# Kernel optimization log

Hardware: AMD Instinct MI355X
Metric: run time of the kernel (lower is better)

Reference implementation:

```python
import jax, jax.numpy as jnp
import numpy as np

B, N, D, S, K = 32, 2048, 512, 2, 1024
DS = D // S  # slice_dim = 256
BETA = 0.25


def setup_inputs() -> dict:
    key = jax.random.key(0)
    k1, k2 = jax.random.split(key)
    h = jax.random.normal(k1, (B, N, D), dtype=jnp.float32)
    # torch init: uniform(-1/K, 1/K) per codebook
    W = jax.random.uniform(k2, (S, K, DS), dtype=jnp.float32,
                           minval=-1.0 / K, maxval=1.0 / K)
    return {"h": h, "W": W}


def reference(h, W):
    Bb, Nn, Dd = h.shape
    Ss, Kk, Ds = W.shape
    # [S, B*N, Ds] sliced views of h
    x = h.reshape(Bb * Nn, Ss, Ds).transpose(1, 0, 2)
    # squared euclidean distances per slice: [S, BN, K]
    x_sq = jnp.sum(x * x, axis=-1, keepdims=True)
    w_sq = jnp.sum(W * W, axis=-1)  # [S, K]
    dist = x_sq + w_sq[:, None, :] - 2.0 * jnp.einsum('smd,skd->smk', x, W)
    ids = jnp.argmin(dist, axis=-1)  # [S, BN]
    # gather codebook vectors per slice
    z_q = jax.vmap(lambda w, i: w[i])(W, ids)  # [S, BN, Ds]
    # per-slice VQ losses (mean over BN*Ds elements), summed over slices
    cb = jnp.mean((z_q - jax.lax.stop_gradient(x)) ** 2, axis=(1, 2))
    cm = jnp.mean((x - jax.lax.stop_gradient(z_q)) ** 2, axis=(1, 2))
    vq_total = jnp.sum(cb + BETA * cm)
    # straight-through estimator
    z_st = x + jax.lax.stop_gradient(z_q - x)  # [S, BN, Ds]
    z = z_st.transpose(1, 0, 2).reshape(Bb, Nn, Dd)
    # pack slice ids: offsets = [1, K, K^2, ...]
    offs = (Kk ** jnp.arange(Ss)).astype(jnp.int32)
    ids_packed = jnp.sum(ids.astype(jnp.int32) * offs[:, None], axis=0).reshape(Bb, Nn)
    return z, ids_packed, vq_total
```

## Files before the change

### kernel.cpp

```cpp
#include <hip/hip_runtime.h>

#define BN_   65536
#define K_    1024
#define DS_   256
#define D_    512
#define TM    64
#define TK    128

__global__ __launch_bounds__(256)
void wsq_kernel(const float* __restrict__ W, float* __restrict__ wsq) {
  const int k = blockIdx.x * 256 + threadIdx.x;
  const float4* row = (const float4*)(W + (size_t)k * DS_);
  float s0 = 0.f, s1 = 0.f, s2 = 0.f, s3 = 0.f;
#pragma unroll
  for (int i = 0; i < DS_ / 4; ++i) {
    const float4 v = row[i];
    s0 = fmaf(v.x, v.x, s0);
    s1 = fmaf(v.y, v.y, s1);
    s2 = fmaf(v.z, v.z, s2);
    s3 = fmaf(v.w, v.w, s3);
  }
  wsq[k] = (s0 + s1) + (s2 + s3);
}

__global__ __launch_bounds__(256)
void xsq_kernel(const float* __restrict__ h, float* __restrict__ xsq) {
  const int idx = blockIdx.x * 256 + threadIdx.x;
  const int s = idx >> 16;
  const int m = idx & 0xFFFF;
  const float* x = h + (size_t)m * D_ + s * DS_;
  float blk[2];
#pragma unroll
  for (int b = 0; b < 2; ++b) {
    const float* a = x + b * 128;
    float r[8];
#pragma unroll
    for (int j = 0; j < 8; ++j) r[j] = __fmul_rn(a[j], a[j]);
    for (int t = 1; t < 16; ++t) {
#pragma unroll
      for (int j = 0; j < 8; ++j) {
        const float p = __fmul_rn(a[t * 8 + j], a[t * 8 + j]);
        r[j] = __fadd_rn(r[j], p);
      }
    }
    const float s01 = __fadd_rn(r[0], r[1]);
    const float s23 = __fadd_rn(r[2], r[3]);
    const float s45 = __fadd_rn(r[4], r[5]);
    const float s67 = __fadd_rn(r[6], r[7]);
    blk[b] = __fadd_rn(__fadd_rn(s01, s23), __fadd_rn(s45, s67));
  }
  xsq[idx] = __fadd_rn(blk[0], blk[1]);
}

__global__ __launch_bounds__(256, 2)
void argmin_kernel(const float* __restrict__ h, const float* __restrict__ W,
                   const float* __restrict__ wsq, const float* __restrict__ xsq,
                   int* __restrict__ ids, float* __restrict__ partials) {
  __shared__ float xs[DS_][TM];
  __shared__ float wst[32][TK];
  float* candv = &wst[0][0];
  int*   candi = (int*)&wst[8][0];

  const int tid = threadIdx.x;
  const int m0  = blockIdx.x * TM;
  const int s   = blockIdx.y;

  {
    const int m  = tid & 63;
    const int dg = tid >> 6;
    const float* xrow = h + (size_t)(m0 + m) * D_ + s * DS_;
#pragma unroll
    for (int it = 0; it < 16; ++it) {
      const int d = it * 16 + dg * 4;
      const float4 v = *(const float4*)(xrow + d);
      xs[d + 0][m] = v.x;
      xs[d + 1][m] = v.y;
      xs[d + 2][m] = v.z;
      xs[d + 3][m] = v.w;
    }
  }

  const int tx = tid & 15;
  const int ty = tid >> 4;
  const float* __restrict__ wsq_s = wsq + s * K_;
  const float* __restrict__ Wb    = W + (size_t)s * K_ * DS_;

  float Xq[4];
#pragma unroll
  for (int i = 0; i < 4; ++i) Xq[i] = xsq[s * BN_ + m0 + tx * 4 + i];

  const int sk = tid & 127;
  const int sh = tid >> 7;
  const float* wbase = Wb + (size_t)sk * DS_ + sh * 16;

  float4 pre[4];
  {
    const float4* p = (const float4*)wbase;
    pre[0] = p[0]; pre[1] = p[1]; pre[2] = p[2]; pre[3] = p[3];
  }

  float bestv[4];
  int   besti[4];
#pragma unroll
  for (int i = 0; i < 4; ++i) { bestv[i] = 3.4e38f; besti[i] = 0x7fffffff; }

  float acc[4][8];
#pragma unroll
  for (int i = 0; i < 4; ++i)
#pragma unroll
    for (int j = 0; j < 8; ++j) acc[i][j] = 0.f;

  for (int c = 0; c < 64; ++c) {
    const int dc = c & 7;
    __syncthreads();
    {
      const float* pf = (const float*)pre;
#pragma unroll
      for (int t = 0; t < 16; ++t) wst[sh * 16 + t][sk] = pf[t];
    }
    __syncthreads();
    {
      const int cn  = (c < 63) ? c + 1 : 63;
      const float4* p = (const float4*)(wbase +
          (size_t)((cn >> 3) * TK) * DS_ + (cn & 7) * 32);
      pre[0] = p[0]; pre[1] = p[1]; pre[2] = p[2]; pre[3] = p[3];
    }

    float acct[4][8];
#pragma unroll
    for (int i = 0; i < 4; ++i)
#pragma unroll
      for (int j = 0; j < 8; ++j) acct[i][j] = 0.f;

#pragma unroll
    for (int d = 0; d < 32; ++d) {
      const float4 a  = *(const float4*)&xs[dc * 32 + d][tx * 4];
      const float4 b0 = *(const float4*)&wst[d][ty * 8];
      const float4 b1 = *(const float4*)&wst[d][ty * 8 + 4];
      const float av[4] = {a.x, a.y, a.z, a.w};
      const float bv[8] = {b0.x, b0.y, b0.z, b0.w, b1.x, b1.y, b1.z, b1.w};
#pragma unroll
      for (int i = 0; i < 4; ++i)
#pragma unroll
        for (int j = 0; j < 8; ++j)
          acct[i][j] = fmaf(av[i], bv[j], acct[i][j]);
    }
#pragma unroll
    for (int i = 0; i < 4; ++i)
#pragma unroll
      for (int j = 0; j < 8; ++j) acc[i][j] += acct[i][j];

    if (dc == 7) {
      const int k0 = (c >> 3) * TK;
#pragma unroll
      for (int i = 0; i < 4; ++i) {
#pragma unroll
        for (int j = 0; j < 8; ++j) {
          const int kk = k0 + ty * 8 + j;
          const float t1 = __fadd_rn(Xq[i], wsq_s[kk]);
          const float dv = __fsub_rn(t1, 2.0f * acc[i][j]);
          if (dv < bestv[i]) { bestv[i] = dv; besti[i] = kk; }
        }
        acc[i][0] = 0.f; acc[i][1] = 0.f; acc[i][2] = 0.f; acc[i][3] = 0.f;
        acc[i][4] = 0.f; acc[i][5] = 0.f; acc[i][6] = 0.f; acc[i][7] = 0.f;
      }
    }
  }

  __syncthreads();
#pragma unroll
  for (int i = 0; i < 4; ++i) {
    candv[ty * TM + tx * 4 + i] = bestv[i];
    candi[ty * TM + tx * 4 + i] = besti[i];
  }
  __syncthreads();
  if (tid < TM) {
    float bv = 3.4e38f;
    int   bi = 0x7fffffff;
#pragma unroll
    for (int t = 0; t < 16; ++t) {
      const float v = candv[t * TM + tid];
      const int   c = candi[t * TM + tid];
      if (v < bv || (v == bv && c < bi)) { bv = v; bi = c; }
    }
    ids[s * BN_ + m0 + tid] = bi;
    float v = bv;
#pragma unroll
    for (int off = 32; off > 0; off >>= 1) v += __shfl_down(v, off);
    if (tid == 0) partials[blockIdx.y * 1024 + blockIdx.x] = v;
  }
}

__global__ __launch_bounds__(256)
void gather_kernel(const float* __restrict__ W, const int* __restrict__ ids,
                   float* __restrict__ out) {
  const int tid = threadIdx.x;
  float* out_ids = out + (size_t)BN_ * D_;
#pragma unroll
  for (int it = 0; it < 4; ++it) {
    const size_t i4 = (size_t)it * 2097152 + (size_t)blockIdx.x * 256 + tid;
    const size_t e  = i4 * 4;
    const int m  = (int)(e >> 9);
    const int d  = (int)(e & 511);
    const int s  = d >> 8;
    const int dd = d & 255;
    const int id = ids[s * BN_ + m];
    const float4 z = *(const float4*)(W + ((size_t)(s * K_ + id)) * DS_ + dd);
    *(float4*)(out + e) = z;
    if (d == 0) {
      const int id1 = ids[BN_ + m];
      out_ids[m] = (float)(id + (id1 << 10));
    }
  }
}

__global__ __launch_bounds__(256)
void finalize_kernel(const float* __restrict__ partials,
                     float* __restrict__ out_vq) {
  __shared__ float red[256];
  const int tid = threadIdx.x;
  float s = 0.f;
  for (int i = tid; i < 2048; i += 256) s += partials[i];
  red[tid] = s;
  __syncthreads();
  for (int off = 128; off > 0; off >>= 1) {
    if (tid < off) red[tid] += red[tid + off];
    __syncthreads();
  }
  if (tid == 0) out_vq[0] = red[0] * (1.25f / 16777216.f);
}

extern "C" void kernel_launch(void* const* d_in, const int* in_sizes, int n_in,
                              void* d_out, int out_size, void* d_ws,
                              size_t ws_size, hipStream_t stream) {
  const float* h = (const float*)d_in[0];
  const float* W = (const float*)d_in[1];
  float* out  = (float*)d_out;
  float* wsf  = (float*)d_ws;
  float* wsq      = wsf;
  float* partials = wsf + 2048;
  int*   ids      = (int*)(wsf + 4096);
  float* xsq      = wsf + 4096 + 131072;

  wsq_kernel<<<8, 256, 0, stream>>>(W, wsq);
  xsq_kernel<<<512, 256, 0, stream>>>(h, xsq);
  argmin_kernel<<<dim3(1024, 2), 256, 0, stream>>>(h, W, wsq, xsq, ids,
                                                   partials);
  gather_kernel<<<8192, 256, 0, stream>>>(W, ids, out);
  finalize_kernel<<<1, 256, 0, stream>>>(partials,
                                         out + (size_t)BN_ * D_ + BN_);
}
```

Baseline: 1.085 ms.

## Pre-transpose codebook and read it directly from global memory in argmin

Adds a kernel that transposes each codebook slice to [D, K] in workspace, falling back to the output buffer if the workspace is too small. The argmin kernel then loads codebook tiles directly from global (L2/L1 cached) memory as float4 instead of staging them through shared memory. This removes two block-wide barriers per chunk and the per-block shared-memory staging, cutting LDS usage, and shared memory is reused for the final candidate reduction. The cost is an extra transpose launch, plus inner-loop operands now depend on global-load latency with no explicit prefetch.

Measured after the change: 1.268 ms. 1.17x slower.

```diff
diff --git a/kernel.cpp b/kernel.cpp
--- a/kernel.cpp
+++ b/kernel.cpp
@@ -52,14 +52,36 @@
   xsq[idx] = __fadd_rn(blk[0], blk[1]);
 }
 
+__global__ __launch_bounds__(256)
+void wt_kernel(const float* __restrict__ W, float* __restrict__ Wt) {
+  __shared__ float t[32][33];
+  const int s  = blockIdx.z;
+  const int kb = blockIdx.x * 32;
+  const int db = blockIdx.y * 32;
+  const int tx = threadIdx.x & 31;
+  const int ty = threadIdx.x >> 5;
+  const float* Ws  = W  + (size_t)s * K_ * DS_;
+  float*       Wts = Wt + (size_t)s * DS_ * K_;
+#pragma unroll
+  for (int i = 0; i < 4; ++i) {
+    const int k = ty + i * 8;
+    t[k][tx] = Ws[(size_t)(kb + k) * DS_ + db + tx];
+  }
+  __syncthreads();
+#pragma unroll
+  for (int i = 0; i < 4; ++i) {
+    const int d = ty + i * 8;
+    Wts[(size_t)(db + d) * K_ + kb + tx] = t[tx][d];
+  }
+}
+
 __global__ __launch_bounds__(256, 2)
-void argmin_kernel(const float* __restrict__ h, const float* __restrict__ W,
+void argmin_kernel(const float* __restrict__ h, const float* __restrict__ Wt,
                    const float* __restrict__ wsq, const float* __restrict__ xsq,
                    int* __restrict__ ids, float* __restrict__ partials) {
   __shared__ float xs[DS_][TM];
-  __shared__ float wst[32][TK];
-  float* candv = &wst[0][0];
-  int*   candi = (int*)&wst[8][0];
+  float* candv = &xs[0][0];
+  int*   candi = (int*)&xs[16][0];
 
   const int tid = threadIdx.x;
   const int m0  = blockIdx.x * TM;
@@ -79,25 +101,16 @@
       xs[d + 3][m] = v.w;
     }
   }
+  __syncthreads();
 
   const int tx = tid & 15;
   const int ty = tid >> 4;
   const float* __restrict__ wsq_s = wsq + s * K_;
-  const float* __restrict__ Wb    = W + (size_t)s * K_ * DS_;
+  const float* __restrict__ Wts   = Wt + (size_t)s * DS_ * K_;
 
   float Xq[4];
 #pragma unroll
   for (int i = 0; i < 4; ++i) Xq[i] = xsq[s * BN_ + m0 + tx * 4 + i];
-
-  const int sk = tid & 127;
-  const int sh = tid >> 7;
-  const float* wbase = Wb + (size_t)sk * DS_ + sh * 16;
-
-  float4 pre[4];
-  {
-    const float4* p = (const float4*)wbase;
-    pre[0] = p[0]; pre[1] = p[1]; pre[2] = p[2]; pre[3] = p[3];
-  }
 
   float bestv[4];
   int   besti[4];
@@ -110,60 +123,49 @@
 #pragma unroll
     for (int j = 0; j < 8; ++j) acc[i][j] = 0.f;
 
-  for (int c = 0; c < 64; ++c) {
-    const int dc = c & 7;
-    __syncthreads();
-    {
-      const float* pf = (const float*)pre;
-#pragma unroll
-      for (int t = 0; t < 16; ++t) wst[sh * 16 + t][sk] = pf[t];
-    }
-    __syncthreads();
-    {
-      const int cn  = (c < 63) ? c + 1 : 63;
-      const float4* p = (const float4*)(wbase +
-          (size_t)((cn >> 3) * TK) * DS_ + (cn & 7) * 32);
-      pre[0] = p[0]; pre[1] = p[1]; pre[2] = p[2]; pre[3] = p[3];
-    }
-
-    float acct[4][8];
-#pragma unroll
-    for (int i = 0; i < 4; ++i)
-#pragma unroll
-      for (int j = 0; j < 8; ++j) acct[i][j] = 0.f;
-
-#pragma unroll
-    for (int d = 0; d < 32; ++d) {
-      const float4 a  = *(const float4*)&xs[dc * 32 + d][tx * 4];
-      const float4 b0 = *(const float4*)&wst[d][ty * 8];
-      const float4 b1 = *(const float4*)&wst[d][ty * 8 + 4];
-      const float av[4] = {a.x, a.y, a.z, a.w};
-      const float bv[8] = {b0.x, b0.y, b0.z, b0.w, b1.x, b1.y, b1.z, b1.w};
+  for (int kt = 0; kt < 8; ++kt) {
+    const int kbase = kt * TK + ty * 8;
+#pragma unroll 1
+    for (int dc = 0; dc < 8; ++dc) {
+      float acct[4][8];
 #pragma unroll
       for (int i = 0; i < 4; ++i)
 #pragma unroll
-        for (int j = 0; j < 8; ++j)
-          acct[i][j] = fmaf(av[i], bv[j], acct[i][j]);
-    }
-#pragma unroll
-    for (int i = 0; i < 4; ++i)
-#pragma unroll
-      for (int j = 0; j < 8; ++j) acc[i][j] += acct[i][j];
-
-    if (dc == 7) {
-      const int k0 = (c >> 3) * TK;
-#pragma unroll
-      for (int i = 0; i < 4; ++i) {
-#pragma unroll
-        for (int j = 0; j < 8; ++j) {
-          const int kk = k0 + ty * 8 + j;
-          const float t1 = __fadd_rn(Xq[i], wsq_s[kk]);
-          const float dv = __fsub_rn(t1, 2.0f * acc[i][j]);
-          if (dv < bestv[i]) { bestv[i] = dv; besti[i] = kk; }
-        }
-        acc[i][0] = 0.f; acc[i][1] = 0.f; acc[i][2] = 0.f; acc[i][3] = 0.f;
-        acc[i][4] = 0.f; acc[i][5] = 0.f; acc[i][6] = 0.f; acc[i][7] = 0.f;
+        for (int j = 0; j < 8; ++j) acct[i][j] = 0.f;
+
+      int woff = (dc * 32) * K_ + kbase;
+#pragma unroll
+      for (int d = 0; d < 32; ++d) {
+        const float4 a  = *(const float4*)&xs[dc * 32 + d][tx * 4];
+        const float4 b0 = *(const float4*)(Wts + woff);
+        const float4 b1 = *(const float4*)(Wts + woff + 4);
+        woff += K_;
+        const float av[4] = {a.x, a.y, a.z, a.w};
+        const float bv[8] = {b0.x, b0.y, b0.z, b0.w, b1.x, b1.y, b1.z, b1.w};
+#pragma unroll
+        for (int i = 0; i < 4; ++i)
+#pragma unroll
+          for (int j = 0; j < 8; ++j)
+            acct[i][j] = fmaf(av[i], bv[j], acct[i][j]);
       }
+#pragma unroll
+      for (int i = 0; i < 4; ++i)
+#pragma unroll
+        for (int j = 0; j < 8; ++j) acc[i][j] += acct[i][j];
+    }
+
+    const int k0 = kt * TK;
+#pragma unroll
+    for (int i = 0; i < 4; ++i) {
+#pragma unroll
+      for (int j = 0; j < 8; ++j) {
+        const int kk = k0 + ty * 8 + j;
+        const float t1 = __fadd_rn(Xq[i], wsq_s[kk]);
+        const float dv = __fsub_rn(t1, 2.0f * acc[i][j]);
+        if (dv < bestv[i]) { bestv[i] = dv; besti[i] = kk; }
+      }
+      acc[i][0] = 0.f; acc[i][1] = 0.f; acc[i][2] = 0.f; acc[i][3] = 0.f;
+      acc[i][4] = 0.f; acc[i][5] = 0.f; acc[i][6] = 0.f; acc[i][7] = 0.f;
     }
   }
 
@@ -241,10 +243,14 @@
   float* partials = wsf + 2048;
   int*   ids      = (int*)(wsf + 4096);
   float* xsq      = wsf + 4096 + 131072;
+  const size_t wt_off = 4096 + 131072 + 131072;
+  float* Wt = (ws_size >= (wt_off + 524288) * sizeof(float))
+                  ? (wsf + wt_off) : out;
 
   wsq_kernel<<<8, 256, 0, stream>>>(W, wsq);
   xsq_kernel<<<512, 256, 0, stream>>>(h, xsq);
-  argmin_kernel<<<dim3(1024, 2), 256, 0, stream>>>(h, W, wsq, xsq, ids,
+  wt_kernel<<<dim3(32, 8, 2), 256, 0, stream>>>(W, Wt);
+  argmin_kernel<<<dim3(1024, 2), 256, 0, stream>>>(h, Wt, wsq, xsq, ids,
                                                    partials);
   gather_kernel<<<8192, 256, 0, stream>>>(W, ids, out);
   finalize_kernel<<<1, 256, 0, stream>>>(partials,
```
